# Kernel optimization log

Hardware: AMD Instinct MI355X
Metric: run time of the kernel (lower is better)

The kernel has to match this reference:

```python
import jax, jax.numpy as jnp
import numpy as np
import math

NUM_HEADS = 16
D_EMBED = 1024
D_HEAD = D_EMBED // NUM_HEADS


def setup_inputs() -> dict:
    key = jax.random.key(0)
    k1, k2, k3 = jax.random.split(key, 3)
    B, S = 4, 2048
    x = jax.random.normal(k1, (B, S, D_EMBED), dtype=jnp.float32)
    # Kaiming-ish init for the fused QKV and output projections
    scale_in = 1.0 / math.sqrt(D_EMBED)
    in_proj_weight = jax.random.normal(k2, (3 * D_EMBED, D_EMBED), dtype=jnp.float32) * scale_in
    out_proj_weight = jax.random.normal(k3, (D_EMBED, D_EMBED), dtype=jnp.float32) * scale_in
    return {
        "x": x,
        "in_proj_weight": in_proj_weight,
        "out_proj_weight": out_proj_weight,
        "causal_mask": 1,
    }


def reference(x, in_proj_weight, out_proj_weight, causal_mask):
    B, S, D = x.shape
    # fused QKV projection: x @ W_in^T -> [B, S, 3D], then split
    qkv = jnp.einsum("bsd,ed->bse", x, in_proj_weight)
    q, k, v = jnp.split(qkv, 3, axis=-1)
    # [B, S, H, dh] -> [B, H, S, dh]
    def to_heads(t):
        return t.reshape(B, S, NUM_HEADS, D_HEAD).transpose(0, 2, 1, 3)
    q, k, v = to_heads(q), to_heads(k), to_heads(v)
    # scores: [B, H, S, S]
    scores = jnp.einsum("bhqd,bhkd->bhqk", q, k) / math.sqrt(D_HEAD)
    if causal_mask:
        mask = jnp.triu(jnp.ones((S, S), dtype=bool), k=1)
        scores = jnp.where(mask, -jnp.inf, scores)
    attn = jax.nn.softmax(scores, axis=-1)
    out = jnp.einsum("bhqk,bhkd->bhqd", attn, v)
    out = out.transpose(0, 2, 1, 3).reshape(B, S, D)
    return jnp.einsum("bsd,ed->bse", out, out_proj_weight)
```

## Files before the change

kernel.cpp:

```cpp
#include <hip/hip_runtime.h>
#include <hip/hip_bf16.h>
#include <stdint.h>

typedef unsigned short u16;
typedef __attribute__((ext_vector_type(8))) short short8;
typedef __attribute__((ext_vector_type(4))) float floatx4;
typedef __attribute__((ext_vector_type(16))) float floatx16;
typedef __attribute__((ext_vector_type(4))) unsigned uint4v;
typedef __attribute__((ext_vector_type(2))) unsigned uint2v;

#define DEV static __device__ __forceinline__

DEV u16 f2bf(float f) {
  __hip_bfloat16 h = __float2bfloat16(f);
  return __builtin_bit_cast(u16, h);
}

DEV float fexp2(float x) {
  float r;
  asm("v_exp_f32 %0, %1" : "=v"(r) : "v"(x));
  return r;
}

DEV unsigned cvtpk(float lo, float hi) {
  unsigned r;
  asm("v_cvt_pk_bf16_f32 %0, %1, %2" : "=v"(r) : "v"(lo), "v"(hi));
  return r;
}

DEV void pswap(unsigned& a, unsigned& b) {
  uint2v r = __builtin_amdgcn_permlane32_swap(a, b, false, false);
  a = r[0];
  b = r[1];
}

DEV void cross32(float v, float& x, float& y) {
  unsigned a = __builtin_bit_cast(unsigned, v), b = a;
  pswap(a, b);
  x = __builtin_bit_cast(float, a);
  y = __builtin_bit_cast(float, b);
}

DEV floatx4 mfma16(short8 a, short8 b, floatx4 c) {
  return __builtin_amdgcn_mfma_f32_16x16x32_bf16(a, b, c, 0, 0, 0);
}
DEV floatx16 mfma32(short8 a, short8 b, floatx16 c) {
  return __builtin_amdgcn_mfma_f32_32x32x16_bf16(a, b, c, 0, 0, 0);
}

DEV void gload_lds16(const void* g, void* l) {
  __builtin_amdgcn_global_load_lds(
      (void __attribute__((address_space(1)))*)(g),
      (void __attribute__((address_space(3)))*)(l),
      16, 0, 0);
}

__global__ void cast3_kernel(const float* __restrict__ x, const float* __restrict__ win,
                             const float* __restrict__ wout,
                             u16* __restrict__ xb, u16* __restrict__ winb,
                             u16* __restrict__ woutb) {
  int i = blockIdx.x * 256 + threadIdx.x;
  const float* src;
  u16* dst;
  int off;
  if (i < 2097152) {
    src = x; dst = xb; off = i;
  } else if (i < 2883584) {
    src = win; dst = winb; off = i - 2097152;
  } else {
    src = wout; dst = woutb; off = i - 2883584;
  }
  float4 v = reinterpret_cast<const float4*>(src)[off];
  ushort4 o;
  o.x = f2bf(v.x); o.y = f2bf(v.y); o.z = f2bf(v.z); o.w = f2bf(v.w);
  reinterpret_cast<ushort4*>(dst)[off] = o;
}

template <int MODE>
__global__ __launch_bounds__(512, 2)
void gemm_bt(const u16* __restrict__ A, const u16* __restrict__ W,
             int M, int N, int K,
             u16* __restrict__ Qb, u16* __restrict__ Kb, u16* __restrict__ Vb,
             float* __restrict__ C) {
  __shared__ u16 As[3][128 * 32];
  __shared__ u16 Bs[3][256 * 32];
  const int tid = threadIdx.x;
  const int wave = tid >> 6, lane = tid & 63;
  const int lr = lane & 15, lg = lane >> 4;
  const int m0 = blockIdx.y * 128, n0 = blockIdx.x * 256;
  const int mq0 = (wave >> 2) * 64, nq0 = (wave & 3) * 64;
  const int swz2 = ((lr >> 1) & 3) * 8;

  floatx4 acc[4][4];
#pragma unroll
  for (int i = 0; i < 4; ++i)
#pragma unroll
    for (int j = 0; j < 4; ++j) acc[i][j] = (floatx4)0.f;

  const int NT = K >> 5;

  auto stage = [&](int t, int bi) {
    {
      int s = tid;
      int row = s >> 2, kc = s & 3;
      int col = (kc ^ ((row >> 1) & 3)) * 8;
      gload_lds16(&A[(size_t)(m0 + row) * K + t * 32 + col], &As[bi][(size_t)s * 8]);
    }
#pragma unroll
    for (int i = 0; i < 2; ++i) {
      int s = tid + i * 512;
      int row = s >> 2, kc = s & 3;
      int col = (kc ^ ((row >> 1) & 3)) * 8;
      gload_lds16(&W[(size_t)(n0 + row) * K + t * 32 + col], &Bs[bi][(size_t)s * 8]);
    }
  };

  stage(0, 0);
  stage(1, 1);

  int bi = 0;
  for (int t = 0; t < NT; ++t) {
    if (t < NT - 1) {
      asm volatile("s_waitcnt vmcnt(3)" ::: "memory");
    } else {
      asm volatile("s_waitcnt vmcnt(0)" ::: "memory");
    }
    __builtin_amdgcn_sched_barrier(0);
    __builtin_amdgcn_s_barrier();
    __builtin_amdgcn_sched_barrier(0);

    int b2 = bi + 2; if (b2 >= 3) b2 -= 3;
    if (t + 2 < NT) stage(t + 2, b2);

    short8 af[4], bf[4];
#pragma unroll
    for (int m = 0; m < 4; ++m)
      af[m] = *reinterpret_cast<const short8*>(
          &As[bi][(mq0 + m * 16 + lr) * 32 + (lg * 8 ^ swz2)]);
#pragma unroll
    for (int nn = 0; nn < 4; ++nn)
      bf[nn] = *reinterpret_cast<const short8*>(
          &Bs[bi][(nq0 + nn * 16 + lr) * 32 + (lg * 8 ^ swz2)]);

    __builtin_amdgcn_s_setprio(1);
#pragma unroll
    for (int i = 0; i < 4; ++i)
#pragma unroll
      for (int j = 0; j < 4; ++j)
        acc[i][j] = mfma16(af[i], bf[j], acc[i][j]);
    __builtin_amdgcn_s_setprio(0);

    if (++bi == 3) bi = 0;
  }

  if (MODE == 0) {
#pragma unroll
    for (int j = 0; j < 4; ++j) {
      int n = n0 + nq0 + j * 16 + lr;
      int which = n >> 10;
      int d = n & 1023;
      int h = d >> 6, dh = d & 63;
      u16* dst = (which == 0) ? Qb : ((which == 1) ? Kb : Vb);
      float scale = (which == 0) ? 0.18033688f : 1.0f;
#pragma unroll
      for (int i = 0; i < 4; ++i) {
#pragma unroll
        for (int r = 0; r < 4; ++r) {
          int m = m0 + mq0 + i * 16 + lg * 4 + r;
          int b = m >> 11, s = m & 2047;
          dst[((size_t)(b * 16 + h) * 2048 + s) * 64 + dh] = f2bf(acc[i][j][r] * scale);
        }
      }
    }
  } else {
#pragma unroll
    for (int i = 0; i < 4; ++i)
#pragma unroll
      for (int j = 0; j < 4; ++j)
#pragma unroll
        for (int r = 0; r < 4; ++r) {
          int m = m0 + mq0 + i * 16 + lg * 4 + r;
          int n = n0 + nq0 + j * 16 + lr;
          C[(size_t)m * N + n] = acc[i][j][r];
        }
  }
}

__global__ __launch_bounds__(256, 2)
void attn_kernel(const u16* __restrict__ Qb, const u16* __restrict__ Kb,
                 const u16* __restrict__ Vb, u16* __restrict__ Ob) {
  const int bh = blockIdx.y;
  const u16* Qh = Qb + (size_t)bh * 2048 * 64;
  const u16* Kh = Kb + (size_t)bh * 2048 * 64;
  const u16* Vh = Vb + (size_t)bh * 2048 * 64;

  __shared__ u16 smem[3][8192];

  const int tid = threadIdx.x, wave = tid >> 6, lane = tid & 63;
  const int ln31 = lane & 31, hi = lane >> 5;
  const int swz = (lane & 7) * 8;
  const int b = bh >> 4, h = bh & 15;

  const int vp = tid & 31, vc8 = tid >> 5;

  auto stage_k = [&](int kvbase, u16* buf) {
#pragma unroll
    for (int i = 0; i < 2; ++i) {
      int s = i * 256 + tid;
      int row = s >> 3;
      int col = ((s & 7) ^ (row & 7)) * 8;
      gload_lds16(&Kh[(size_t)(kvbase + row) * 64 + col], &buf[(size_t)s * 8]);
    }
  };
  auto load_v = [&](int kvbase, short8& v0, short8& v1) {
    v0 = *reinterpret_cast<const short8*>(&Vh[(size_t)(kvbase + 2 * vp) * 64 + vc8 * 8]);
    v1 = *reinterpret_cast<const short8*>(&Vh[(size_t)(kvbase + 2 * vp + 1) * 64 + vc8 * 8]);
  };
  auto write_v = [&](u16* buf, short8 v0, short8 v1) {
#pragma unroll
    for (int j = 0; j < 8; ++j) {
      int d = vc8 * 8 + j;
      uint32_t pk = (uint32_t)(u16)v0[j] | ((uint32_t)(u16)v1[j] << 16);
      *reinterpret_cast<uint32_t*>(&buf[4096 + d * 64 + ((2 * vp) ^ ((d & 7) * 8))]) = pk;
    }
  };

  for (int ph = 0; ph < 2; ++ph) {
    const int tq = ph ? (15 - (int)blockIdx.x) : (int)blockIdx.x;
    const int q0w = tq * 128 + wave * 32;
    const int qrow = q0w + ln31;

    short8 qf[4];
#pragma unroll
    for (int c = 0; c < 4; ++c)
      qf[c] = *reinterpret_cast<const short8*>(
          &Qh[(size_t)qrow * 64 + c * 16 + hi * 8]);

    floatx16 accO0 = (floatx16)0.f, accO1 = (floatx16)0.f;
    float m_run = -1e30f, l_run = 0.f;

    auto do_qk = [&](int kvq, floatx16& SQ0, floatx16& SQ1, const u16* Ksq) {
      if (kvq > q0w + 31) return;
      SQ0 = (floatx16)0.f;
      SQ1 = (floatx16)0.f;
      __builtin_amdgcn_s_setprio(1);
#pragma unroll
      for (int c = 0; c < 4; ++c) {
        short8 kfA = *reinterpret_cast<const short8*>(
            &Ksq[ln31 * 64 + ((c * 16 + hi * 8) ^ swz)]);
        short8 kfB = *reinterpret_cast<const short8*>(
            &Ksq[(32 + ln31) * 64 + ((c * 16 + hi * 8) ^ swz)]);
        SQ0 = mfma32(kfA, qf[c], SQ0);
        SQ1 = mfma32(kfB, qf[c], SQ1);
      }
      __builtin_amdgcn_s_setprio(0);
    };

    auto do_smpv = [&](int kv0_, floatx16& SS0, floatx16& SS1, const u16* bufv) {
      if (kv0_ > q0w + 31) return;
      if (kv0_ + 63 > q0w) {
#pragma unroll
        for (int reg = 0; reg < 16; ++reg) {
          int kvA = kv0_ + (reg & 3) + 8 * (reg >> 2) + 4 * hi;
          if (kvA > qrow) SS0[reg] = -1e30f;
          if (kvA + 32 > qrow) SS1[reg] = -1e30f;
        }
      }
      float m8[8];
#pragma unroll
      for (int i = 0; i < 8; ++i)
        m8[i] = fmaxf(fmaxf(SS0[i], SS0[i + 8]), fmaxf(SS1[i], SS1[i + 8]));
      float mx = fmaxf(fmaxf(fmaxf(m8[0], m8[1]), fmaxf(m8[2], m8[3])),
                       fmaxf(fmaxf(m8[4], m8[5]), fmaxf(m8[6], m8[7])));
      {
        float xa, xb;
        cross32(mx, xa, xb);
        mx = fmaxf(xa, xb);
      }
      bool small_ = (mx <= m_run + 8.f);
      if (!__all(small_)) {
        float mn = fmaxf(m_run, mx);
        float fac = fexp2(m_run - mn);
        m_run = mn;
        l_run *= fac;
        accO0 *= fac;
        accO1 *= fac;
      }
#pragma unroll
      for (int i = 0; i < 16; ++i) SS0[i] = fexp2(SS0[i] - m_run);
#pragma unroll
      for (int i = 0; i < 16; ++i) SS1[i] = fexp2(SS1[i] - m_run);
      float a8[8];
#pragma unroll
      for (int i = 0; i < 8; ++i)
        a8[i] = (SS0[i] + SS0[i + 8]) + (SS1[i] + SS1[i + 8]);
      float rs = ((a8[0] + a8[1]) + (a8[2] + a8[3])) + ((a8[4] + a8[5]) + (a8[6] + a8[7]));
      {
        float xa, xb;
        cross32(rs, xa, xb);
        rs = xa + xb;
      }
      l_run += rs;
      short8 pf[4];
#define BUILD_PF(idx, S, base)                                        \
      {                                                               \
        unsigned u01 = cvtpk(S[base + 0], S[base + 1]);               \
        unsigned u23 = cvtpk(S[base + 2], S[base + 3]);               \
        unsigned u45 = cvtpk(S[base + 4], S[base + 5]);               \
        unsigned u67 = cvtpk(S[base + 6], S[base + 7]);               \
        pswap(u01, u45);                                              \
        pswap(u23, u67);                                              \
        uint4v w; w.x = u01; w.y = u23; w.z = u45; w.w = u67;         \
        pf[idx] = __builtin_bit_cast(short8, w);                      \
      }
      BUILD_PF(0, SS0, 0)
      BUILD_PF(1, SS0, 8)
      BUILD_PF(2, SS1, 0)
      BUILD_PF(3, SS1, 8)
#undef BUILD_PF
      const u16* Vt = bufv + 4096;
      __builtin_amdgcn_s_setprio(1);
#pragma unroll
      for (int c = 0; c < 4; ++c) {
        short8 vfA = *reinterpret_cast<const short8*>(
            &Vt[ln31 * 64 + ((c * 16 + hi * 8) ^ swz)]);
        short8 vfB = *reinterpret_cast<const short8*>(
            &Vt[(32 + ln31) * 64 + ((c * 16 + hi * 8) ^ swz)]);
        accO0 = mfma32(vfA, pf[c], accO0);
        accO1 = mfma32(vfB, pf[c], accO1);
      }
      __builtin_amdgcn_s_setprio(0);
    };

    const int nt = 2 * (tq + 1);

    __syncthreads();
    stage_k(0, smem[0]);
    {
      short8 v0, v1;
      load_v(0, v0, v1);
      write_v(smem[0], v0, v1);
    }
    stage_k(64, smem[1]);
    {
      short8 v0, v1;
      load_v(64, v0, v1);
      write_v(smem[1], v0, v1);
    }
    __syncthreads();

    floatx16 SA0, SA1, SB0, SB1;
    do_qk(0, SA0, SA1, smem[0]);

    for (int it = 0; it < nt; it += 2) {
      {
        const int kvc = it * 64;
        short8 nv0, nv1;
        const bool do_st = (it + 2) < nt;
        u16* sbuf = smem[(it + 2) % 3];
        if (do_st) {
          stage_k(kvc + 128, sbuf);
          load_v(kvc + 128, nv0, nv1);
        }
        do_qk(kvc + 64, SB0, SB1, smem[(it + 1) % 3]);
        do_smpv(kvc, SA0, SA1, smem[it % 3]);
        if (do_st) write_v(sbuf, nv0, nv1);
        __syncthreads();
      }
      {
        const int kvc = it * 64 + 64;
        short8 nv0, nv1;
        const bool do_st = (it + 3) < nt;
        u16* sbuf = smem[(it + 3) % 3];
        if (do_st) {
          stage_k(kvc + 128, sbuf);
          load_v(kvc + 128, nv0, nv1);
        }
        if (it + 2 < nt) do_qk(kvc + 64, SA0, SA1, smem[(it + 2) % 3]);
        do_smpv(kvc, SB0, SB1, smem[(it + 1) % 3]);
        if (do_st) write_v(sbuf, nv0, nv1);
        __syncthreads();
      }
    }

    u16* ep = &smem[0][0] + wave * 2048;
    float inv = 1.0f / l_run;
#define EPI_W(ACC, dh2)                                               \
    {                                                                 \
      _Pragma("unroll")                                               \
      for (int rp = 0; rp < 8; ++rp) {                                \
        int reg = rp * 2;                                             \
        unsigned pk = cvtpk(ACC[reg] * inv, ACC[reg + 1] * inv);      \
        int d = dh2 * 32 + (reg & 3) + 8 * (reg >> 2) + 4 * hi;       \
        *reinterpret_cast<uint32_t*>(                                 \
            &ep[ln31 * 64 + (d ^ ((ln31 & 7) * 8))]) = pk;            \
      }                                                               \
    }
    EPI_W(accO0, 0)
    EPI_W(accO1, 1)
#undef EPI_W
#pragma unroll
    for (int g = 0; g < 4; ++g) {
      int d0 = hi * 32 + g * 8;
      short8 o8 = *reinterpret_cast<const short8*>(
          &ep[ln31 * 64 + (d0 ^ ((ln31 & 7) * 8))]);
      *reinterpret_cast<short8*>(
          &Ob[(size_t)(b * 2048 + q0w + ln31) * 1024 + h * 64 + d0]) = o8;
    }
  }
}

extern "C" void kernel_launch(void* const* d_in, const int* in_sizes, int n_in,
                              void* d_out, int out_size, void* d_ws, size_t ws_size,
                              hipStream_t stream) {
  const float* x    = (const float*)d_in[0];
  const float* win  = (const float*)d_in[1];
  const float* wout = (const float*)d_in[2];
  float* out = (float*)d_out;

  char* ws = (char*)d_ws;
  u16* xb    = (u16*)(ws + 0);
  u16* winb  = (u16*)(ws + 16777216);
  u16* woutb = (u16*)(ws + 23068672);
  u16* Qb    = (u16*)(ws + 25165824);
  u16* Kb    = (u16*)(ws + 41943040);
  u16* Vb    = (u16*)(ws + 58720256);
  u16* Ob    = (u16*)(ws + 75497472);

  cast3_kernel<<<12288, 256, 0, stream>>>(x, win, wout, xb, winb, woutb);

  gemm_bt<0><<<dim3(12, 64), 512, 0, stream>>>(xb, winb, 8192, 3072, 1024,
                                               Qb, Kb, Vb, nullptr);
  attn_kernel<<<dim3(8, 64), 256, 0, stream>>>(Qb, Kb, Vb, Ob);
  gemm_bt<1><<<dim3(4, 64), 512, 0, stream>>>(Ob, woutb, 8192, 1024, 1024,
                                              nullptr, nullptr, nullptr, out);
}
```

Measured before the change: 178.5 us.

## Double GEMM K-tile to 64 and split each tile into two interleaved MFMA phases

The GEMM K step grows from 32 to 64, so LDS buffers double and the XOR swizzle changes to an 8-chunk pattern. Each iteration now runs two halves. The first half loads the A fragments and half of the B fragments, issues the A and first B global-to-LDS prefetch, then runs MFMAs. After an extra barrier, the second half loads the rest of B, issues the remaining prefetch, and runs more MFMAs. The aim is to halve barrier and loop overhead per unit of K and to spread global-load issue among the MFMAs. In exchange, LDS use is 3x48KB = 144KB per block, which may reduce occupancy below the launch-bounds target of 2, and an extra barrier is added per iteration.

```diff
diff --git a/kernel.cpp b/kernel.cpp
--- a/kernel.cpp
+++ b/kernel.cpp
@@ -82,14 +82,13 @@
              int M, int N, int K,
              u16* __restrict__ Qb, u16* __restrict__ Kb, u16* __restrict__ Vb,
              float* __restrict__ C) {
-  __shared__ u16 As[3][128 * 32];
-  __shared__ u16 Bs[3][256 * 32];
+  __shared__ u16 As[3][128 * 64];
+  __shared__ u16 Bs[3][256 * 64];
   const int tid = threadIdx.x;
   const int wave = tid >> 6, lane = tid & 63;
   const int lr = lane & 15, lg = lane >> 4;
   const int m0 = blockIdx.y * 128, n0 = blockIdx.x * 256;
   const int mq0 = (wave >> 2) * 64, nq0 = (wave & 3) * 64;
-  const int swz2 = ((lr >> 1) & 3) * 8;
 
   floatx4 acc[4][4];
 #pragma unroll
@@ -97,31 +96,36 @@
 #pragma unroll
     for (int j = 0; j < 4; ++j) acc[i][j] = (floatx4)0.f;
 
-  const int NT = K >> 5;
-
-  auto stage = [&](int t, int bi) {
-    {
-      int s = tid;
-      int row = s >> 2, kc = s & 3;
-      int col = (kc ^ ((row >> 1) & 3)) * 8;
-      gload_lds16(&A[(size_t)(m0 + row) * K + t * 32 + col], &As[bi][(size_t)s * 8]);
-    }
+  const int NT = K >> 6;
+
+  auto stage_a = [&](int t, int bi) {
 #pragma unroll
     for (int i = 0; i < 2; ++i) {
-      int s = tid + i * 512;
-      int row = s >> 2, kc = s & 3;
-      int col = (kc ^ ((row >> 1) & 3)) * 8;
-      gload_lds16(&W[(size_t)(n0 + row) * K + t * 32 + col], &Bs[bi][(size_t)s * 8]);
+      int s = i * 512 + tid;
+      int row = s >> 3;
+      int col = ((s & 7) ^ (row & 7)) * 8;
+      gload_lds16(&A[(size_t)(m0 + row) * K + t * 64 + col], &As[bi][(size_t)s * 8]);
     }
   };
-
-  stage(0, 0);
-  stage(1, 1);
+  auto stage_b = [&](int t, int bi, int i0, int i1) {
+#pragma unroll 4
+    for (int i = i0; i < i1; ++i) {
+      int s = i * 512 + tid;
+      int row = s >> 3;
+      int col = ((s & 7) ^ (row & 7)) * 8;
+      gload_lds16(&W[(size_t)(n0 + row) * K + t * 64 + col], &Bs[bi][(size_t)s * 8]);
+    }
+  };
+
+  stage_a(0, 0);
+  stage_b(0, 0, 0, 4);
+  stage_a(1, 1);
+  stage_b(1, 1, 0, 4);
 
   int bi = 0;
   for (int t = 0; t < NT; ++t) {
     if (t < NT - 1) {
-      asm volatile("s_waitcnt vmcnt(3)" ::: "memory");
+      asm volatile("s_waitcnt vmcnt(6)" ::: "memory");
     } else {
       asm volatile("s_waitcnt vmcnt(0)" ::: "memory");
     }
@@ -130,25 +134,63 @@
     __builtin_amdgcn_sched_barrier(0);
 
     int b2 = bi + 2; if (b2 >= 3) b2 -= 3;
-    if (t + 2 < NT) stage(t + 2, b2);
-
-    short8 af[4], bf[4];
-#pragma unroll
-    for (int m = 0; m < 4; ++m)
-      af[m] = *reinterpret_cast<const short8*>(
-          &As[bi][(mq0 + m * 16 + lr) * 32 + (lg * 8 ^ swz2)]);
-#pragma unroll
-    for (int nn = 0; nn < 4; ++nn)
-      bf[nn] = *reinterpret_cast<const short8*>(
-          &Bs[bi][(nq0 + nn * 16 + lr) * 32 + (lg * 8 ^ swz2)]);
-
+    const bool do_st = (t + 2 < NT);
+
+    short8 af[4][2], bf01[2][2];
+#pragma unroll
+    for (int i = 0; i < 4; ++i) {
+      int row = mq0 + i * 16 + lr;
+#pragma unroll
+      for (int kh = 0; kh < 2; ++kh)
+        af[i][kh] = *reinterpret_cast<const short8*>(
+            &As[bi][row * 64 + (((kh * 4 + lg) ^ (row & 7)) * 8)]);
+    }
+#pragma unroll
+    for (int j = 0; j < 2; ++j) {
+      int row = nq0 + j * 16 + lr;
+#pragma unroll
+      for (int kh = 0; kh < 2; ++kh)
+        bf01[j][kh] = *reinterpret_cast<const short8*>(
+            &Bs[bi][row * 64 + (((kh * 4 + lg) ^ (row & 7)) * 8)]);
+    }
+    if (do_st) {
+      stage_a(t + 2, b2);
+      stage_b(t + 2, b2, 0, 1);
+    }
+    __builtin_amdgcn_sched_barrier(0);
     __builtin_amdgcn_s_setprio(1);
 #pragma unroll
-    for (int i = 0; i < 4; ++i)
-#pragma unroll
-      for (int j = 0; j < 4; ++j)
-        acc[i][j] = mfma16(af[i], bf[j], acc[i][j]);
+    for (int kh = 0; kh < 2; ++kh)
+#pragma unroll
+      for (int i = 0; i < 4; ++i)
+#pragma unroll
+        for (int j = 0; j < 2; ++j)
+          acc[i][j] = mfma16(af[i][kh], bf01[j][kh], acc[i][j]);
     __builtin_amdgcn_s_setprio(0);
+    __builtin_amdgcn_sched_barrier(0);
+    __builtin_amdgcn_s_barrier();
+
+    short8 bf23[2][2];
+#pragma unroll
+    for (int j = 0; j < 2; ++j) {
+      int row = nq0 + (j + 2) * 16 + lr;
+#pragma unroll
+      for (int kh = 0; kh < 2; ++kh)
+        bf23[j][kh] = *reinterpret_cast<const short8*>(
+            &Bs[bi][row * 64 + (((kh * 4 + lg) ^ (row & 7)) * 8)]);
+    }
+    if (do_st) stage_b(t + 2, b2, 1, 4);
+    __builtin_amdgcn_sched_barrier(0);
+    __builtin_amdgcn_s_setprio(1);
+#pragma unroll
+    for (int kh = 0; kh < 2; ++kh)
+#pragma unroll
+      for (int i = 0; i < 4; ++i)
+#pragma unroll
+        for (int j = 0; j < 2; ++j)
+          acc[i][j + 2] = mfma16(af[i][kh], bf23[j][kh], acc[i][j + 2]);
+    __builtin_amdgcn_s_setprio(0);
+    __builtin_amdgcn_sched_barrier(0);
 
     if (++bi == 3) bi = 0;
   }
```

After: 164.8 us, median of 2. 7.7% less time.
